# Optimization experiments

Measured on AMD Instinct MI355X. Metric: run time of the kernel, lower is better.

## Reference

```python
import jax, jax.numpy as jnp
import numpy as np

B, Q, K, D, H = 8, 1024, 1024, 1024, 16
HD = D // H
FFN = 4 * D


def layer_norm(x, w, b, eps=1e-5):
    mu = jnp.mean(x, axis=-1, keepdims=True)
    var = jnp.var(x, axis=-1, keepdims=True)
    return (x - mu) * jax.lax.rsqrt(var + eps) * w + b


def setup_inputs() -> dict:
    key = jax.random.key(0)
    ks = jax.random.split(key, 10)
    query = jax.random.normal(ks[0], (B, Q, D), dtype=jnp.float32)
    key_value = jax.random.normal(ks[1], (B, K, D), dtype=jnp.float32)
    kpm = jax.random.randint(ks[2], (B, K), 0, 2).astype(bool)
    kpm = kpm.at[:, 0].set(True)  # guarantee >=1 valid key per row
    s = 0.02
    return {
        "query": query,
        "key_value": key_value,
        "key_padding_mask": kpm,
        "ln_q_w": jnp.ones((D,), jnp.float32), "ln_q_b": jnp.zeros((D,), jnp.float32),
        "ln_kv_w": jnp.ones((D,), jnp.float32), "ln_kv_b": jnp.zeros((D,), jnp.float32),
        "ln_f_w": jnp.ones((D,), jnp.float32), "ln_f_b": jnp.zeros((D,), jnp.float32),
        "in_proj_w": jax.random.normal(ks[3], (3 * D, D), jnp.float32) * s,
        "in_proj_b": jnp.zeros((3 * D,), jnp.float32),
        "out_proj_w": jax.random.normal(ks[4], (D, D), jnp.float32) * s,
        "out_proj_b": jnp.zeros((D,), jnp.float32),
        "ffn_w1": jax.random.normal(ks[5], (FFN, D), jnp.float32) * s,
        "ffn_b1": jnp.zeros((FFN,), jnp.float32),
        "ffn_w2": jax.random.normal(ks[6], (D, FFN), jnp.float32) * s,
        "ffn_b2": jnp.zeros((D,), jnp.float32),
    }


def reference(query, key_value, key_padding_mask,
              ln_q_w, ln_q_b, ln_kv_w, ln_kv_b, ln_f_w, ln_f_b,
              in_proj_w, in_proj_b, out_proj_w, out_proj_b,
              ffn_w1, ffn_b1, ffn_w2, ffn_b2):
    q_norm = layer_norm(query, ln_q_w, ln_q_b)
    kv_norm = layer_norm(key_value, ln_kv_w, ln_kv_b)

    Wq, Wk, Wv = jnp.split(in_proj_w, 3, axis=0)
    bq, bk, bv = jnp.split(in_proj_b, 3, axis=0)
    q = (q_norm @ Wq.T + bq).reshape(B, Q, H, HD).transpose(0, 2, 1, 3)  # (B,H,Q,hd)
    k = (kv_norm @ Wk.T + bk).reshape(B, K, H, HD).transpose(0, 2, 1, 3)
    v = (kv_norm @ Wv.T + bv).reshape(B, K, H, HD).transpose(0, 2, 1, 3)

    scale = 1.0 / jnp.sqrt(jnp.float32(HD))
    scores = jnp.einsum('bhqd,bhkd->bhqk', q * scale, k)  # (B,H,Q,K)
    scores = jnp.where(key_padding_mask[:, None, None, :], scores, -jnp.inf)
    attn = jax.nn.softmax(scores, axis=-1)

    attn_out = jnp.einsum('bhqk,bhkd->bhqd', attn, v)
    attn_out = attn_out.transpose(0, 2, 1, 3).reshape(B, Q, D)
    attn_out = attn_out @ out_proj_w.T + out_proj_b

    x = query + attn_out
    h = layer_norm(x, ln_f_w, ln_f_b)
    h = jax.nn.gelu(h @ ffn_w1.T + ffn_b1, approximate=False)
    x = x + (h @ ffn_w2.T + ffn_b2)

    attn_weights = jnp.mean(attn, axis=1)  # average over heads -> (B,Q,K)
    return x, attn_weights
```

## Files before the change

### kernel.cpp

```cpp
#include <hip/hip_runtime.h>
#include <math.h>

typedef short  s16x8 __attribute__((ext_vector_type(8)));
typedef short  s16x4 __attribute__((ext_vector_type(4)));
typedef float  f32x4 __attribute__((ext_vector_type(4)));

#define DEV static __device__ __forceinline__
#define M0SHIFT 3.0f

DEV float b2f(unsigned short h) {
    unsigned int u = ((unsigned int)h) << 16;
    float f; __builtin_memcpy(&f, &u, 4); return f;
}
DEV unsigned short f2b(float f) {
    unsigned int u; __builtin_memcpy(&u, &f, 4);
    unsigned int r = (u + 0x7fffu + ((u >> 16) & 1u)) >> 16;
    return (unsigned short)r;
}
DEV unsigned fb(float x) { unsigned u; __builtin_memcpy(&u, &x, 4); return u; }
DEV s16x4 pack4(float a0, float a1, float a2, float a3) {
    unsigned lo = __builtin_amdgcn_perm(fb(a1), fb(a0), 0x07060302u);
    unsigned hi = __builtin_amdgcn_perm(fb(a3), fb(a2), 0x07060302u);
    unsigned long long p = ((unsigned long long)hi << 32) | lo;
    s16x4 r; __builtin_memcpy(&r, &p, 8); return r;
}

#define GLD16(gp, lp) __builtin_amdgcn_global_load_lds( \
    (const __attribute__((address_space(1))) unsigned int*)(const void*)(gp), \
    (__attribute__((address_space(3))) unsigned int*)(void*)(lp), 16, 0, 0)

#if __has_builtin(__builtin_amdgcn_mfma_f32_16x16x16_bf16)
#define MFMA16(a, b, c) __builtin_amdgcn_mfma_f32_16x16x16_bf16(a, b, c, 0, 0, 0)
#else
#define MFMA16(a, b, c) __builtin_amdgcn_mfma_f32_16x16x16bf16_1k(a, b, c, 0, 0, 0)
#endif

DEV float ldsel(const void* p, size_t i, bool f32) {
    return f32 ? ((const float*)p)[i] : b2f(((const unsigned short*)p)[i]);
}
DEV s16x8 ld8sel(const void* p, size_t eidx, bool f32) {
    if (f32) {
        const float* f = (const float*)p + eidx;
        f32x4 a = *(const f32x4*)f;
        f32x4 b = *(const f32x4*)(f + 4);
        s16x8 o;
        o[0]=(short)f2b(a[0]); o[1]=(short)f2b(a[1]); o[2]=(short)f2b(a[2]); o[3]=(short)f2b(a[3]);
        o[4]=(short)f2b(b[0]); o[5]=(short)f2b(b[1]); o[6]=(short)f2b(b[2]); o[7]=(short)f2b(b[3]);
        return o;
    }
    return *(const s16x8*)((const unsigned short*)p + eidx);
}

__global__ __launch_bounds__(256) void dtype_probe(
    const unsigned int* __restrict__ q, int* __restrict__ flag)
{
    int t = threadIdx.x;
    int hits = 0;
    for (int i = t; i < 2048; i += 256) {
        unsigned e0 = (q[i] >> 7) & 0xFFu;
        hits += (e0 >= 0x70u && e0 <= 0x87u) ? 1 : 0;
    }
#pragma unroll
    for (int m = 32; m >= 1; m >>= 1) hits += __shfl_xor(hits, m);
    __shared__ int sh[4];
    if ((t & 63) == 0) sh[t >> 6] = hits;
    __syncthreads();
    if (t == 0) *flag = (sh[0] + sh[1] + sh[2] + sh[3] > 1024) ? 0 : 1;
}

__global__ __launch_bounds__(1024) void mask_prep(
    const unsigned int* __restrict__ w, const unsigned char* __restrict__ bytes,
    float* __restrict__ mf)
{
    __shared__ int flag;
    const int t = threadIdx.x;
    if (t == 0) flag = 0;
    __syncthreads();
    unsigned int a = w[t], b = w[t + 1024];
    if (a > 1u || b > 1u) flag = 1;
    __syncthreads();
    const int f = flag;
    const float NEGINF = -__builtin_inff();
#pragma unroll
    for (int i = 0; i < 8; i++) {
        int c = t * 8 + i;
        int v = f ? (int)(bytes[c] != 0) : (int)(w[c] != 0);
        mf[c] = v ? -M0SHIFT : NEGINF;
    }
}

struct CvtArgs { const void* s[8]; };
__global__ __launch_bounds__(256) void cvt_w(
    const int* __restrict__ flagp, CvtArgs a, unsigned short* __restrict__ dst)
{
    const int f = *flagp;
    size_t e = ((size_t)blockIdx.x * 256 + threadIdx.x) * 8;
    if (e >= 12592128u) return;
    const size_t off[9] = {0u, 3145728u, 4194304u, 8388608u, 12582912u,
                           12585984u, 12587008u, 12591104u, 12592128u};
    int s = 0;
    while (e >= off[s + 1]) s++;
    *(s16x8*)&dst[e] = ld8sel(a.s[s], e - off[s], f == 1);
}

__global__ __launch_bounds__(256) void ln_k(
    const int* __restrict__ flagp, int xmode, int wmode,
    const void* __restrict__ x1p, const void* __restrict__ w1p, const void* __restrict__ b1p,
    unsigned short* __restrict__ y1p,
    const void* __restrict__ x2p, const void* __restrict__ w2p, const void* __restrict__ b2p,
    unsigned short* __restrict__ y2p)
{
    const int f = *flagp;
    const bool xf = (xmode == 2) ? (f == 1) : (xmode == 1);
    const bool wf = (wmode == 2) ? (f == 1) : (wmode == 1);
    int row = blockIdx.x;
    const void* x = x1p; const void* wgt = w1p; const void* bias = b1p;
    unsigned short* y = y1p;
    if (x2p && row >= 8192) {
        row -= 8192; x = x2p; wgt = w2p; bias = b2p; y = y2p;
    }
    const int t = threadIdx.x;
    const int w = t >> 6, lane = t & 63;
    float f0, f1, f2, f3;
    if (xf) {
        f32x4 v = *(const f32x4*)((const float*)x + (size_t)row * 1024 + t * 4);
        f0 = v[0]; f1 = v[1]; f2 = v[2]; f3 = v[3];
    } else {
        s16x4 v = *(const s16x4*)((const unsigned short*)x + (size_t)row * 1024 + t * 4);
        f0 = b2f((unsigned short)v[0]); f1 = b2f((unsigned short)v[1]);
        f2 = b2f((unsigned short)v[2]); f3 = b2f((unsigned short)v[3]);
    }
    __shared__ float red[4];
    float s = f0 + f1 + f2 + f3;
#pragma unroll
    for (int m = 32; m >= 1; m >>= 1) s += __shfl_xor(s, m);
    if (lane == 0) red[w] = s;
    __syncthreads();
    float mu = (red[0] + red[1] + red[2] + red[3]) * (1.0f / 1024.0f);
    float d0 = f0 - mu, d1 = f1 - mu, d2 = f2 - mu, d3 = f3 - mu;
    float q = d0 * d0 + d1 * d1 + d2 * d2 + d3 * d3;
#pragma unroll
    for (int m = 32; m >= 1; m >>= 1) q += __shfl_xor(q, m);
    __syncthreads();
    if (lane == 0) red[w] = q;
    __syncthreads();
    float var = (red[0] + red[1] + red[2] + red[3]) * (1.0f / 1024.0f);
    float rs = rsqrtf(var + 1e-5f);
    s16x4 vo;
    vo[0] = (short)f2b(d0 * rs * ldsel(wgt, t*4+0, wf) + ldsel(bias, t*4+0, wf));
    vo[1] = (short)f2b(d1 * rs * ldsel(wgt, t*4+1, wf) + ldsel(bias, t*4+1, wf));
    vo[2] = (short)f2b(d2 * rs * ldsel(wgt, t*4+2, wf) + ldsel(bias, t*4+2, wf));
    vo[3] = (short)f2b(d3 * rs * ldsel(wgt, t*4+3, wf) + ldsel(bias, t*4+3, wf));
    *(s16x4*)&y[(size_t)row * 1024 + t * 4] = vo;
}

__global__ __launch_bounds__(256) void gemm_bt(
    const int* __restrict__ flagp,
    const unsigned short* __restrict__ A,
    const void* __restrict__ W, size_t woff, int wmode,
    const void* __restrict__ bias, size_t boff, int bmode,
    const void* __restrict__ res, int rmode,
    void* __restrict__ C, int omode,
    int M, int N, int Kd, int ldw, int ldc, int act)
{
    const int f = *flagp;
    const bool wf = (wmode == 2) && (f == 1);
    __shared__ alignas(16) unsigned short As[128 * 32];
    __shared__ alignas(16) unsigned short Bs[128 * 32];
    const int t = threadIdx.x;
    const int m0 = blockIdx.y * 128, n0 = blockIdx.x * 128;
    const int w = t >> 6, lane = t & 63, quad = lane >> 4, l16 = lane & 15;
    const int wm = (w >> 1) * 64, wn = (w & 1) * 64;
    const f32x4 zero = {0.f, 0.f, 0.f, 0.f};
    f32x4 acc[4][4];
#pragma unroll
    for (int i = 0; i < 4; i++)
#pragma unroll
        for (int j = 0; j < 4; j++) acc[i][j] = zero;
    const int r0 = t >> 2, c0 = (t & 3) * 8;
    unsigned short* AsW = As + (size_t)w * 512;
    unsigned short* BsW = Bs + (size_t)w * 512;
    const unsigned short* W16 = (const unsigned short*)W + woff;
    const float*          W32 = (const float*)W + woff;

    for (int kt = 0; kt < Kd; kt += 32) {
        GLD16(&A[(size_t)(m0 + r0) * Kd + kt + c0],      AsW);
        GLD16(&A[(size_t)(m0 + r0 + 64) * Kd + kt + c0], AsW + 2048);
        if (wf) {
            *(s16x8*)&Bs[r0 * 32 + c0]        = ld8sel(W32, (size_t)(n0 + r0) * ldw + kt + c0, true);
            *(s16x8*)&Bs[(r0 + 64) * 32 + c0] = ld8sel(W32, (size_t)(n0 + r0 + 64) * ldw + kt + c0, true);
        } else {
            GLD16(&W16[(size_t)(n0 + r0) * ldw + kt + c0],      BsW);
            GLD16(&W16[(size_t)(n0 + r0 + 64) * ldw + kt + c0], BsW + 2048);
        }
        __syncthreads();
        s16x8 af[4], bfr[4];
#pragma unroll
        for (int i = 0; i < 4; i++) {
            af[i]  = *(const s16x8*)&As[(wm + i * 16 + l16) * 32 + quad * 8];
            bfr[i] = *(const s16x8*)&Bs[(wn + i * 16 + l16) * 32 + quad * 8];
        }
#pragma unroll
        for (int mi = 0; mi < 4; mi++)
#pragma unroll
            for (int ni = 0; ni < 4; ni++)
                acc[mi][ni] = __builtin_amdgcn_mfma_f32_16x16x32_bf16(af[mi], bfr[ni], acc[mi][ni], 0, 0, 0);
        __syncthreads();
    }
    const bool bf = (bmode == 2) && (f == 1);
    const bool rf = (rmode == 2) || (rmode == 3 && f == 1);
    const bool of = (omode == 1) || (omode == 2 && f == 1);
#pragma unroll
    for (int mi = 0; mi < 4; mi++)
#pragma unroll
        for (int ni = 0; ni < 4; ni++)
#pragma unroll
            for (int r = 0; r < 4; r++) {
                int gr = m0 + wm + mi * 16 + quad * 4 + r;
                int gc = n0 + wn + ni * 16 + l16;
                float v = acc[mi][ni][r];
                if (bmode >= 0) v += ldsel(bias, boff + gc, bf);
                if (act) v = 0.5f * v * (1.f + erff(v * 0.70710678118f));
                if (rmode) v += ldsel(res, (size_t)gr * ldc + gc, rf);
                size_t ci = (size_t)gr * ldc + gc;
                if (of) ((float*)C)[ci] = v;
                else ((unsigned short*)C)[ci] = f2b(v);
            }
}

__global__ __launch_bounds__(512, 2) void gemm8(
    const unsigned short* __restrict__ A,
    const unsigned short* __restrict__ W, size_t woff,
    const unsigned short* __restrict__ bias, size_t boff,
    unsigned short* __restrict__ C,
    int Kd, int ldc, int act)
{
    __shared__ alignas(16) unsigned short lds[65536];
    const unsigned short* Wp = W + woff;
    const int t = threadIdx.x;
    const int w = t >> 6, lane = t & 63, quad = lane >> 4, l16 = lane & 15;
    const int wr = w >> 2, wcn = w & 3;

    const int gx = (int)gridDim.x;
    const int nwg = gx * (int)gridDim.y;
    const int lid = (int)blockIdx.y * gx + (int)blockIdx.x;
    const int swz = (lid & 7) * (nwg >> 3) + (lid >> 3);
    const int m0 = (swz / gx) * 256, n0 = (swz % gx) * 256;

    const int hrow = w * 16 + (lane >> 3);
    const int scol = ((lane & 7) ^ ((lane & 32) ? 2 : 0)) * 8;
    const int NT = Kd >> 6;

    const int swq = (l16 & 4) ? 16 : 0;
    const int ck0 = (quad * 8) ^ swq;
    const int ck1 = (32 + quad * 8) ^ swq;

    const f32x4 zero = {0.f, 0.f, 0.f, 0.f};
    f32x4 acc[8][4];
#pragma unroll
    for (int i = 0; i < 8; i++)
#pragma unroll
        for (int j = 0; j < 4; j++) acc[i][j] = zero;
    s16x8 aF[4][2], bLo[2][2], bHi[2][2];

#define SA8(bb,h,tt,g) GLD16(&A[(size_t)(m0 + (h)*128 + hrow + (g)*8) * Kd + (size_t)(tt)*64 + scol], \
                             &lds[(bb)*32768 + (h)*8192 + (w*16 + (g)*8)*64])
#define SB8(bb,h,tt,g) GLD16(&Wp[(size_t)(n0 + (h)*128 + hrow + (g)*8) * Kd + (size_t)(tt)*64 + scol], \
                             &lds[(bb)*32768 + 16384 + (h)*8192 + (w*16 + (g)*8)*64])
#define LDA8(bb,q) { _Pragma("unroll") for (int i_ = 0; i_ < 4; i_++) { \
        const int ar_ = (q)*128 + wr*64 + i_*16 + l16; \
        aF[i_][0] = *(const s16x8*)&lds[(bb)*32768 + ar_*64 + ck0]; \
        aF[i_][1] = *(const s16x8*)&lds[(bb)*32768 + ar_*64 + ck1]; } }
#define LDB8(bb,dst,q) { _Pragma("unroll") for (int j_ = 0; j_ < 2; j_++) { \
        const int br_ = (q)*128 + wcn*32 + j_*16 + l16; \
        dst[j_][0] = *(const s16x8*)&lds[(bb)*32768 + 16384 + br_*64 + ck0]; \
        dst[j_][1] = *(const s16x8*)&lds[(bb)*32768 + 16384 + br_*64 + ck1]; } }
#define MM8(mq,nq,bsrc) { __builtin_amdgcn_s_setprio(1); \
        _Pragma("unroll") for (int i_ = 0; i_ < 4; i_++) \
        _Pragma("unroll") for (int j_ = 0; j_ < 2; j_++) { \
            acc[(mq)*4+i_][(nq)*2+j_] = __builtin_amdgcn_mfma_f32_16x16x32_bf16(aF[i_][0], bsrc[j_][0], acc[(mq)*4+i_][(nq)*2+j_], 0, 0, 0); \
            acc[(mq)*4+i_][(nq)*2+j_] = __builtin_amdgcn_mfma_f32_16x16x32_bf16(aF[i_][1], bsrc[j_][1], acc[(mq)*4+i_][(nq)*2+j_], 0, 0, 0); } \
        __builtin_amdgcn_s_setprio(0); }
#define BAR8() __builtin_amdgcn_s_barrier()
#define VMW8(n) asm volatile("s_waitcnt vmcnt(" #n ")" ::: "memory")

    SA8(0, 0, 0, 0); SA8(0, 0, 0, 1);
    SB8(0, 0, 0, 0); SB8(0, 0, 0, 1);
    SB8(0, 1, 0, 0); SB8(0, 1, 0, 1);
    SA8(0, 1, 0, 0); SA8(0, 1, 0, 1);
    VMW8(4); BAR8();

    for (int tt = 0; tt < NT - 1; tt++) {
        const int bb = tt & 1, nb = bb ^ 1;
        SA8(nb, 0, tt + 1, 0); SA8(nb, 0, tt + 1, 1);
        LDA8(bb, 0); LDB8(bb, bLo, 0);
        MM8(0, 0, bLo);
        VMW8(4); BAR8();
        SB8(nb, 0, tt + 1, 0); SB8(nb, 0, tt + 1, 1);
        LDB8(bb, bHi, 1);
        MM8(0, 1, bHi);
        VMW8(4); BAR8();
        SB8(nb, 1, tt + 1, 0); SB8(nb, 1, tt + 1, 1);
        LDA8(bb, 1);
        MM8(1, 1, bHi);
        BAR8();
        SA8(nb, 1, tt + 1, 0); SA8(nb, 1, tt + 1, 1);
        MM8(1, 0, bLo);
        VMW8(4); BAR8();
    }
    {
        const int bb = (NT - 1) & 1;
        LDA8(bb, 0); LDB8(bb, bLo, 0); MM8(0, 0, bLo); VMW8(2); BAR8();
        LDB8(bb, bHi, 1);              MM8(0, 1, bHi); VMW8(0); BAR8();
        LDA8(bb, 1);                   MM8(1, 1, bHi);
        MM8(1, 0, bLo);
    }

#pragma unroll
    for (int nq = 0; nq < 2; nq++)
#pragma unroll
    for (int j = 0; j < 2; j++) {
        const int gc = n0 + nq * 128 + wcn * 32 + j * 16 + l16;
        const float bv = b2f(bias[boff + gc]);
#pragma unroll
        for (int mq = 0; mq < 2; mq++)
#pragma unroll
        for (int i = 0; i < 4; i++)
#pragma unroll
        for (int r = 0; r < 4; r++) {
            const int gr = m0 + mq * 128 + wr * 64 + i * 16 + quad * 4 + r;
            float v = acc[mq * 4 + i][nq * 2 + j][r] + bv;
            if (act) v = 0.5f * v * (1.f + erff(v * 0.70710678118f));
            C[(size_t)gr * ldc + gc] = f2b(v);
        }
    }
#undef SA8
#undef SB8
#undef LDA8
#undef LDB8
#undef MM8
#undef BAR8
#undef VMW8
}

__global__ __launch_bounds__(256) void repack_kv(
    const unsigned short* __restrict__ kvp,
    unsigned short* __restrict__ kf, unsigned short* __restrict__ vf)
{
    const bool isv = blockIdx.x >= 4096;
    int t = (blockIdx.x - (isv ? 4096 : 0)) * 256 + threadIdx.x;
    int lane = t & 63;
    int quad = lane >> 4, l16 = lane & 15;
    if (!isv) {
        int half = (t >> 6) & 1, tile = (t >> 7) & 63;
        int h = (t >> 13) & 15, b = t >> 17;
        s16x8 v = *(const s16x8*)&kvp[(size_t)(b * 1024 + tile * 16 + l16) * 2048
                                      + h * 64 + half * 32 + quad * 8];
        *(s16x8*)&kf[(size_t)t * 8] = v;
    } else {
        int dt = (t >> 6) & 3, kt5 = (t >> 8) & 31;
        int h = (t >> 13) & 15, b = t >> 17;
        int d = dt * 16 + l16;
        s16x8 o;
#pragma unroll
        for (int j = 0; j < 8; j++) {
            int k = kt5 * 32 + ((j < 4) ? (quad * 4 + j) : (16 + quad * 4 + j - 4));
            o[j] = (short)kvp[(size_t)(b * 1024 + k) * 2048 + 1024 + h * 64 + d];
        }
        *(s16x8*)&vf[(size_t)t * 8] = o;
    }
}

__global__ __launch_bounds__(256) void flash_attn(
    const unsigned short* __restrict__ qp, const unsigned short* __restrict__ kf,
    const unsigned short* __restrict__ vf, const float* __restrict__ maskf,
    unsigned short* __restrict__ ao, float* __restrict__ ml)
{
    const int bh = blockIdx.x;
    const int b = bh >> 4, h = bh & 15;
    const int t = threadIdx.x, w = t >> 6, lane = t & 63, quad = lane >> 4, l16 = lane & 15;
    const int q0 = (blockIdx.y * 4 + w) * 16;
    const f32x4 zero = {0.f, 0.f, 0.f, 0.f};

    const unsigned short* kfb = kf + (size_t)bh * 65536;
    const unsigned short* vfb = vf + (size_t)bh * 65536;

    const size_t qbase = (size_t)(b * 1024 + q0 + l16) * 1024 + h * 64 + quad * 8;
    s16x8 qf0 = *(const s16x8*)&qp[qbase];
    s16x8 qf1 = *(const s16x8*)&qp[qbase + 32];

    f32x4 O[4];
#pragma unroll
    for (int dt = 0; dt < 4; dt++) O[dt] = zero;
    float l_s = 0.f;

    for (int kt = 0; kt < 1024; kt += 32) {
        const int tile2 = (kt >> 4) * 2;
        s16x8 k00 = *(const s16x8*)&kfb[(size_t)(tile2 + 0) * 512 + lane * 8];
        s16x8 k01 = *(const s16x8*)&kfb[(size_t)(tile2 + 1) * 512 + lane * 8];
        s16x8 k10 = *(const s16x8*)&kfb[(size_t)(tile2 + 2) * 512 + lane * 8];
        s16x8 k11 = *(const s16x8*)&kfb[(size_t)(tile2 + 3) * 512 + lane * 8];
        f32x4 St0 = __builtin_amdgcn_mfma_f32_16x16x32_bf16(k00, qf0, zero, 0, 0, 0);
        St0 = __builtin_amdgcn_mfma_f32_16x16x32_bf16(k01, qf1, St0, 0, 0, 0);
        f32x4 St1 = __builtin_amdgcn_mfma_f32_16x16x32_bf16(k10, qf0, zero, 0, 0, 0);
        St1 = __builtin_amdgcn_mfma_f32_16x16x32_bf16(k11, qf1, St1, 0, 0, 0);

        f32x4 mk0 = *(const f32x4*)&maskf[b * 1024 + kt + quad * 4];
        f32x4 mk1 = *(const f32x4*)&maskf[b * 1024 + kt + 16 + quad * 4];
        float x0[4], x1[4];
#pragma unroll
        for (int r = 0; r < 4; r++) {
            x0[r] = __expf(St0[r] * 0.125f + mk0[r]);
            x1[r] = __expf(St1[r] * 0.125f + mk1[r]);
        }
        float rs = (x0[0] + x0[1]) + (x0[2] + x0[3])
                 + (x1[0] + x1[1]) + (x1[2] + x1[3]);
        rs += __shfl_xor(rs, 16);
        rs += __shfl_xor(rs, 32);
        l_s += rs;

        s16x4 p0 = pack4(x0[0], x0[1], x0[2], x0[3]);
        s16x4 p1 = pack4(x1[0], x1[1], x1[2], x1[3]);
        const size_t vrow = (size_t)(kt >> 5) * 4;
#pragma unroll
        for (int dt = 0; dt < 4; dt++) {
            s16x8 vv = *(const s16x8*)&vfb[(vrow + dt) * 512 + lane * 8];
            s16x4 v0 = {vv[0], vv[1], vv[2], vv[3]};
            s16x4 v1 = {vv[4], vv[5], vv[6], vv[7]};
            O[dt] = MFMA16(p0, v0, O[dt]);
            O[dt] = MFMA16(p1, v1, O[dt]);
        }
    }
    float li = (l_s > 0.f) ? 1.f / l_s : 0.f;
    float lib[4];
#pragma unroll
    for (int r = 0; r < 4; r++) lib[r] = __shfl(li, quad * 4 + r);
#pragma unroll
    for (int dt = 0; dt < 4; dt++)
#pragma unroll
        for (int r = 0; r < 4; r++) {
            int qrow = q0 + quad * 4 + r;
            ao[(size_t)(b * 1024 + qrow) * 1024 + h * 64 + dt * 16 + l16] = f2b(O[dt][r] * lib[r]);
        }
    if (lane < 16) {
        size_t ix = ((size_t)(b * 16 + h) * 1024 + q0 + l16) * 2;
        ml[ix] = M0SHIFT; ml[ix + 1] = l_s;
    }
}

__global__ __launch_bounds__(256) void attn_mean_k(
    const int* __restrict__ flagp,
    const unsigned short* __restrict__ qp, const unsigned short* __restrict__ kf,
    const float* __restrict__ maskf, const float* __restrict__ ml,
    void* __restrict__ dout)
{
    const bool of = (*flagp == 1);
    const size_t SHIFT = (size_t)8 * 1024 * 1024;
    const int b = blockIdx.x, q0 = blockIdx.y * 16;
    const int t = threadIdx.x, w = t >> 6, lane = t & 63, quad = lane >> 4, l16 = lane & 15;
    const int kbase = w * 256;
    const f32x4 zero = {0.f, 0.f, 0.f, 0.f};
    f32x4 acc[16];
#pragma unroll
    for (int i = 0; i < 16; i++) acc[i] = zero;
    float mka[16];
#pragma unroll
    for (int i = 0; i < 16; i++)
        mka[i] = maskf[b * 1024 + kbase + i * 16 + l16];
    for (int h = 0; h < 16; h++) {
        const size_t qb = (size_t)(b * 1024 + q0 + l16) * 1024 + h * 64 + quad * 8;
        s16x8 a0 = *(const s16x8*)&qp[qb];
        s16x8 a1 = *(const s16x8*)&qp[qb + 32];
        float cexp[4], lirow[4];
#pragma unroll
        for (int r = 0; r < 4; r++) {
            size_t ix = ((size_t)(b * 16 + h) * 1024 + q0 + quad * 4 + r) * 2;
            float lv = ml[ix + 1];
            cexp[r] = M0SHIFT - ml[ix];
            lirow[r] = (lv > 0.f) ? 1.f / lv : 0.f;
        }
        const unsigned short* kfb = kf + ((size_t)(b * 16 + h) * 128 + (kbase >> 4) * 2) * 512;
#pragma unroll
        for (int i = 0; i < 16; i++) {
            s16x8 b0 = *(const s16x8*)&kfb[(size_t)(i * 2 + 0) * 512 + lane * 8];
            s16x8 b1 = *(const s16x8*)&kfb[(size_t)(i * 2 + 1) * 512 + lane * 8];
            f32x4 S = __builtin_amdgcn_mfma_f32_16x16x32_bf16(a0, b0, zero, 0, 0, 0);
            S = __builtin_amdgcn_mfma_f32_16x16x32_bf16(a1, b1, S, 0, 0, 0);
#pragma unroll
            for (int r = 0; r < 4; r++)
                acc[i][r] += __expf(S[r] * 0.125f + mka[i] + cexp[r]) * lirow[r];
        }
    }
#pragma unroll
    for (int i = 0; i < 16; i++)
#pragma unroll
        for (int r = 0; r < 4; r++) {
            int qrow = q0 + quad * 4 + r;
            size_t oi = SHIFT + (size_t)(b * 1024 + qrow) * 1024 + kbase + i * 16 + l16;
            float v = acc[i][r] * 0.0625f;
            if (of) ((float*)dout)[oi] = v;
            else ((unsigned short*)dout)[oi] = f2b(v);
        }
}

extern "C" void kernel_launch(void* const* d_in, const int* in_sizes, int n_in,
                              void* d_out, int out_size, void* d_ws, size_t ws_size,
                              hipStream_t stream) {
    const void* query = d_in[0];
    const void* keyv  = d_in[1];
    const void* maskr = d_in[2];
    const void* lqw = d_in[3];  const void* lqb = d_in[4];
    const void* lkw = d_in[5];  const void* lkb = d_in[6];
    const void* lfw = d_in[7];  const void* lfb = d_in[8];
    const void* ipw = d_in[9];  const void* ipb = d_in[10];
    const void* opw = d_in[11]; const void* opb = d_in[12];
    const void* w1  = d_in[13]; const void* b1  = d_in[14];
    const void* w2  = d_in[15]; const void* b2  = d_in[16];

    char* ws = (char*)d_ws;
    const size_t MB = 1024 * 1024;
    unsigned short* qn  = (unsigned short*)(ws + 0 * MB);
    unsigned short* kvn = (unsigned short*)(ws + 16 * MB);
    unsigned short* qpj = (unsigned short*)(ws + 32 * MB);
    unsigned short* kvp = (unsigned short*)(ws + 48 * MB);
    unsigned short* kfr = (unsigned short*)(ws + 80 * MB);
    unsigned short* vfr = (unsigned short*)(ws + 16 * MB);
    float*          ml  = (float*)(ws + 96 * MB);
    int*            fl  = (int*)(ws + 97 * MB);
    float*          mf  = (float*)(ws + 97 * MB + 256 * 1024);
    unsigned short* aco = (unsigned short*)(ws + 0 * MB);
    float*          xbf = (float*)(ws + 16 * MB);
    unsigned short* hn  = (unsigned short*)(ws + 48 * MB);
    unsigned short* g   = (unsigned short*)(ws + 64 * MB);
    unsigned short* wc  = (unsigned short*)(ws + 98 * MB);

    const bool big = ws_size >= (size_t)125 * MB;
    const size_t cWq = 0, cWk = 1048576, cWo = 3145728;
    const size_t cW1 = 4194304, cW2 = 8388608;
    const size_t cBq = 12582912, cBo = 12585984, cB1 = 12587008, cB2 = 12591104;

    const void *Wq, *Wk, *Wo, *Wf1, *Wf2, *Bq, *Bo, *Bf1, *Bf2;
    size_t wq_o, wk_o, wo_o, w1_o, w2_o, bq_o, bk_o, bo_o, b1_o, b2_o;
    int wm, bm;
    if (big) {
        Wq = Wk = Wo = Wf1 = Wf2 = Bq = Bo = Bf1 = Bf2 = wc;
        wq_o = cWq; wk_o = cWk; wo_o = cWo; w1_o = cW1; w2_o = cW2;
        bq_o = cBq; bk_o = cBq + 1024; bo_o = cBo; b1_o = cB1; b2_o = cB2;
        wm = 0; bm = 0;
    } else {
        Wq = Wk = ipw; Wo = opw; Wf1 = w1; Wf2 = w2;
        Bq = ipb; Bo = opb; Bf1 = b1; Bf2 = b2;
        wq_o = 0; wk_o = 1048576; wo_o = 0; w1_o = 0; w2_o = 0;
        bq_o = 0; bk_o = 1024; bo_o = 0; b1_o = 0; b2_o = 0;
        wm = 2; bm = 2;
    }

    dtype_probe<<<1, 256, 0, stream>>>((const unsigned int*)query, fl);
    mask_prep<<<1, 1024, 0, stream>>>((const unsigned int*)maskr, (const unsigned char*)maskr, mf);
    if (big) {
        CvtArgs ca; ca.s[0] = ipw; ca.s[1] = opw; ca.s[2] = w1; ca.s[3] = w2;
        ca.s[4] = ipb; ca.s[5] = opb; ca.s[6] = b1; ca.s[7] = b2;
        cvt_w<<<6149, 256, 0, stream>>>(fl, ca, wc);
    }

    ln_k<<<16384, 256, 0, stream>>>(fl, 2, 2, query, lqw, lqb, qn, keyv, lkw, lkb, kvn);

    gemm_bt<<<dim3(8, 64), 256, 0, stream>>>(fl, qn,  Wq, wq_o, wm, Bq, bq_o, bm,
                                             nullptr, 0, qpj, 0, 8192, 1024, 1024, 1024, 1024, 0);
    if (big) {
        gemm8<<<dim3(8, 32), 512, 0, stream>>>(kvn, wc, wk_o, wc, bk_o,
                                               kvp, 1024, 2048, 0);
    } else {
        gemm_bt<<<dim3(16, 64), 256, 0, stream>>>(fl, kvn, Wk, wk_o, wm, Bq, bk_o, bm,
                                                  nullptr, 0, kvp, 0, 8192, 2048, 1024, 1024, 2048, 0);
    }

    repack_kv<<<8192, 256, 0, stream>>>(kvp, kfr, vfr);
    flash_attn<<<dim3(128, 16), 256, 0, stream>>>(qpj, kfr, vfr, mf, aco, ml);
    attn_mean_k<<<dim3(8, 64), 256, 0, stream>>>(fl, qpj, kfr, mf, ml, d_out);

    gemm_bt<<<dim3(8, 64), 256, 0, stream>>>(fl, aco, Wo, wo_o, wm, Bo, bo_o, bm,
                                             query, 3, xbf, 1, 8192, 1024, 1024, 1024, 1024, 0);
    ln_k<<<8192, 256, 0, stream>>>(fl, 1, 2, xbf, lfw, lfb, hn,
                                   nullptr, nullptr, nullptr, nullptr);

    if (big) {
        gemm8<<<dim3(8, 32), 512, 0, stream>>>(hn, wc, w1_o, wc, b1_o,
                                               g, 1024, 2048, 1);
    } else {
        gemm_bt<<<dim3(16, 64), 256, 0, stream>>>(fl, hn, Wf1, w1_o, wm, Bf1, b1_o, bm,
                                                  nullptr, 0, g, 0, 8192, 2048, 1024, 1024, 2048, 1);
    }
    gemm_bt<<<dim3(8, 64), 256, 0, stream>>>(fl, g, Wf2, w2_o, wm, Bf2, b2_o, bm,
                                             xbf, 2, xbf, 1, 8192, 1024, 2048, 4096, 1024, 0);
    if (big) {
        gemm8<<<dim3(8, 32), 512, 0, stream>>>(hn, wc, w1_o + (size_t)2048 * 1024, wc, b1_o + 2048,
                                               g, 1024, 2048, 1);
    } else {
        gemm_bt<<<dim3(16, 64), 256, 0, stream>>>(fl, hn, Wf1, w1_o + (size_t)2048 * 1024, wm,
                                                  Bf1, b1_o + 2048, bm,
                                                  nullptr, 0, g, 0, 8192, 2048, 1024, 1024, 2048, 1);
    }
    gemm_bt<<<dim3(8, 64), 256, 0, stream>>>(fl, g, Wf2, w2_o + 2048, wm,
                                             nullptr, 0, -1,
                                             xbf, 2, d_out, 2, 8192, 1024, 2048, 4096, 1024, 0);
}
```

Before: 812.5 us.

## Process two query tiles per wave in flash attention and use exp2

```diff
diff --git a/kernel.cpp b/kernel.cpp
--- a/kernel.cpp
+++ b/kernel.cpp
@@ -7,6 +7,14 @@
 
 #define DEV static __device__ __forceinline__
 #define M0SHIFT 3.0f
+#define LOG2E   1.44269504088896f
+#define SCL2F   0.18033688011112f
+
+#if __has_builtin(__builtin_amdgcn_exp2f)
+#define EXP2F(x) __builtin_amdgcn_exp2f(x)
+#else
+#define EXP2F(x) exp2f(x)
+#endif
 
 DEV float b2f(unsigned short h) {
     unsigned int u = ((unsigned int)h) << 16;
@@ -85,7 +93,7 @@
     for (int i = 0; i < 8; i++) {
         int c = t * 8 + i;
         int v = f ? (int)(bytes[c] != 0) : (int)(w[c] != 0);
-        mf[c] = v ? -M0SHIFT : NEGINF;
+        mf[c] = v ? (-M0SHIFT * LOG2E) : NEGINF;
     }
 }
 
@@ -371,7 +379,7 @@
     }
 }
 
-__global__ __launch_bounds__(256) void flash_attn(
+__global__ __launch_bounds__(256, 4) void flash_attn(
     const unsigned short* __restrict__ qp, const unsigned short* __restrict__ kf,
     const unsigned short* __restrict__ vf, const float* __restrict__ maskf,
     unsigned short* __restrict__ ao, float* __restrict__ ml)
@@ -379,20 +387,21 @@
     const int bh = blockIdx.x;
     const int b = bh >> 4, h = bh & 15;
     const int t = threadIdx.x, w = t >> 6, lane = t & 63, quad = lane >> 4, l16 = lane & 15;
-    const int q0 = (blockIdx.y * 4 + w) * 16;
+    const int q0 = (blockIdx.y * 4 + w) * 32;
     const f32x4 zero = {0.f, 0.f, 0.f, 0.f};
 
     const unsigned short* kfb = kf + (size_t)bh * 65536;
     const unsigned short* vfb = vf + (size_t)bh * 65536;
 
-    const size_t qbase = (size_t)(b * 1024 + q0 + l16) * 1024 + h * 64 + quad * 8;
-    s16x8 qf0 = *(const s16x8*)&qp[qbase];
-    s16x8 qf1 = *(const s16x8*)&qp[qbase + 32];
-
-    f32x4 O[4];
-#pragma unroll
-    for (int dt = 0; dt < 4; dt++) O[dt] = zero;
-    float l_s = 0.f;
+    const size_t qbA = (size_t)(b * 1024 + q0 + l16) * 1024 + h * 64 + quad * 8;
+    const size_t qbB = qbA + (size_t)16 * 1024;
+    s16x8 qa0 = *(const s16x8*)&qp[qbA], qa1 = *(const s16x8*)&qp[qbA + 32];
+    s16x8 qb0 = *(const s16x8*)&qp[qbB], qb1 = *(const s16x8*)&qp[qbB + 32];
+
+    f32x4 OA[4], OB[4];
+#pragma unroll
+    for (int dt = 0; dt < 4; dt++) { OA[dt] = zero; OB[dt] = zero; }
+    float lsA = 0.f, lsB = 0.f;
 
     for (int kt = 0; kt < 1024; kt += 32) {
         const int tile2 = (kt >> 4) * 2;
@@ -400,51 +409,73 @@
         s16x8 k01 = *(const s16x8*)&kfb[(size_t)(tile2 + 1) * 512 + lane * 8];
         s16x8 k10 = *(const s16x8*)&kfb[(size_t)(tile2 + 2) * 512 + lane * 8];
         s16x8 k11 = *(const s16x8*)&kfb[(size_t)(tile2 + 3) * 512 + lane * 8];
-        f32x4 St0 = __builtin_amdgcn_mfma_f32_16x16x32_bf16(k00, qf0, zero, 0, 0, 0);
-        St0 = __builtin_amdgcn_mfma_f32_16x16x32_bf16(k01, qf1, St0, 0, 0, 0);
-        f32x4 St1 = __builtin_amdgcn_mfma_f32_16x16x32_bf16(k10, qf0, zero, 0, 0, 0);
-        St1 = __builtin_amdgcn_mfma_f32_16x16x32_bf16(k11, qf1, St1, 0, 0, 0);
+        const size_t vrow = (size_t)(kt >> 5) * 4;
+        s16x8 vv[4];
+#pragma unroll
+        for (int dt = 0; dt < 4; dt++)
+            vv[dt] = *(const s16x8*)&vfb[(vrow + dt) * 512 + lane * 8];
+
+        f32x4 SA0 = __builtin_amdgcn_mfma_f32_16x16x32_bf16(k00, qa0, zero, 0, 0, 0);
+        SA0 = __builtin_amdgcn_mfma_f32_16x16x32_bf16(k01, qa1, SA0, 0, 0, 0);
+        f32x4 SA1 = __builtin_amdgcn_mfma_f32_16x16x32_bf16(k10, qa0, zero, 0, 0, 0);
+        SA1 = __builtin_amdgcn_mfma_f32_16x16x32_bf16(k11, qa1, SA1, 0, 0, 0);
+        f32x4 SB0 = __builtin_amdgcn_mfma_f32_16x16x32_bf16(k00, qb0, zero, 0, 0, 0);
+        SB0 = __builtin_amdgcn_mfma_f32_16x16x32_bf16(k01, qb1, SB0, 0, 0, 0);
+        f32x4 SB1 = __builtin_amdgcn_mfma_f32_16x16x32_bf16(k10, qb0, zero, 0, 0, 0);
+        SB1 = __builtin_amdgcn_mfma_f32_16x16x32_bf16(k11, qb1, SB1, 0, 0, 0);
 
         f32x4 mk0 = *(const f32x4*)&maskf[b * 1024 + kt + quad * 4];
         f32x4 mk1 = *(const f32x4*)&maskf[b * 1024 + kt + 16 + quad * 4];
-        float x0[4], x1[4];
+        float xA0[4], xA1[4], xB0[4], xB1[4];
 #pragma unroll
         for (int r = 0; r < 4; r++) {
-            x0[r] = __expf(St0[r] * 0.125f + mk0[r]);
-            x1[r] = __expf(St1[r] * 0.125f + mk1[r]);
-        }
-        float rs = (x0[0] + x0[1]) + (x0[2] + x0[3])
-                 + (x1[0] + x1[1]) + (x1[2] + x1[3]);
-        rs += __shfl_xor(rs, 16);
-        rs += __shfl_xor(rs, 32);
-        l_s += rs;
-
-        s16x4 p0 = pack4(x0[0], x0[1], x0[2], x0[3]);
-        s16x4 p1 = pack4(x1[0], x1[1], x1[2], x1[3]);
-        const size_t vrow = (size_t)(kt >> 5) * 4;
+            xA0[r] = EXP2F(SA0[r] * SCL2F + mk0[r]);
+            xA1[r] = EXP2F(SA1[r] * SCL2F + mk1[r]);
+            xB0[r] = EXP2F(SB0[r] * SCL2F + mk0[r]);
+            xB1[r] = EXP2F(SB1[r] * SCL2F + mk1[r]);
+        }
+        float rsA = (xA0[0] + xA0[1]) + (xA0[2] + xA0[3])
+                  + (xA1[0] + xA1[1]) + (xA1[2] + xA1[3]);
+        float rsB = (xB0[0] + xB0[1]) + (xB0[2] + xB0[3])
+                  + (xB1[0] + xB1[1]) + (xB1[2] + xB1[3]);
+        rsA += __shfl_xor(rsA, 16);  rsA += __shfl_xor(rsA, 32);
+        rsB += __shfl_xor(rsB, 16);  rsB += __shfl_xor(rsB, 32);
+        lsA += rsA;  lsB += rsB;
+
+        s16x4 pA0 = pack4(xA0[0], xA0[1], xA0[2], xA0[3]);
+        s16x4 pA1 = pack4(xA1[0], xA1[1], xA1[2], xA1[3]);
+        s16x4 pB0 = pack4(xB0[0], xB0[1], xB0[2], xB0[3]);
+        s16x4 pB1 = pack4(xB1[0], xB1[1], xB1[2], xB1[3]);
 #pragma unroll
         for (int dt = 0; dt < 4; dt++) {
-            s16x8 vv = *(const s16x8*)&vfb[(vrow + dt) * 512 + lane * 8];
-            s16x4 v0 = {vv[0], vv[1], vv[2], vv[3]};
-            s16x4 v1 = {vv[4], vv[5], vv[6], vv[7]};
-            O[dt] = MFMA16(p0, v0, O[dt]);
-            O[dt] = MFMA16(p1, v1, O[dt]);
-        }
-    }
-    float li = (l_s > 0.f) ? 1.f / l_s : 0.f;
-    float lib[4];
-#pragma unroll
-    for (int r = 0; r < 4; r++) lib[r] = __shfl(li, quad * 4 + r);
+            s16x4 v0 = {vv[dt][0], vv[dt][1], vv[dt][2], vv[dt][3]};
+            s16x4 v1 = {vv[dt][4], vv[dt][5], vv[dt][6], vv[dt][7]};
+            OA[dt] = MFMA16(pA0, v0, OA[dt]);
+            OA[dt] = MFMA16(pA1, v1, OA[dt]);
+            OB[dt] = MFMA16(pB0, v0, OB[dt]);
+            OB[dt] = MFMA16(pB1, v1, OB[dt]);
+        }
+    }
+    float liA = (lsA > 0.f) ? 1.f / lsA : 0.f;
+    float liB = (lsB > 0.f) ? 1.f / lsB : 0.f;
+    float libA[4], libB[4];
+#pragma unroll
+    for (int r = 0; r < 4; r++) {
+        libA[r] = __shfl(liA, quad * 4 + r);
+        libB[r] = __shfl(liB, quad * 4 + r);
+    }
 #pragma unroll
     for (int dt = 0; dt < 4; dt++)
 #pragma unroll
         for (int r = 0; r < 4; r++) {
-            int qrow = q0 + quad * 4 + r;
-            ao[(size_t)(b * 1024 + qrow) * 1024 + h * 64 + dt * 16 + l16] = f2b(O[dt][r] * lib[r]);
+            int qrA = q0 + quad * 4 + r;
+            ao[(size_t)(b * 1024 + qrA) * 1024 + h * 64 + dt * 16 + l16] = f2b(OA[dt][r] * libA[r]);
+            ao[(size_t)(b * 1024 + qrA + 16) * 1024 + h * 64 + dt * 16 + l16] = f2b(OB[dt][r] * libB[r]);
         }
     if (lane < 16) {
         size_t ix = ((size_t)(b * 16 + h) * 1024 + q0 + l16) * 2;
-        ml[ix] = M0SHIFT; ml[ix + 1] = l_s;
+        ml[ix] = M0SHIFT;      ml[ix + 1] = lsA;
+        ml[ix + 32] = M0SHIFT; ml[ix + 33] = lsB;
     }
 }
 
@@ -476,7 +507,7 @@
         for (int r = 0; r < 4; r++) {
             size_t ix = ((size_t)(b * 16 + h) * 1024 + q0 + quad * 4 + r) * 2;
             float lv = ml[ix + 1];
-            cexp[r] = M0SHIFT - ml[ix];
+            cexp[r] = (M0SHIFT - ml[ix]) * LOG2E;
             lirow[r] = (lv > 0.f) ? 1.f / lv : 0.f;
         }
         const unsigned short* kfb = kf + ((size_t)(b * 16 + h) * 128 + (kbase >> 4) * 2) * 512;
@@ -488,7 +519,7 @@
             S = __builtin_amdgcn_mfma_f32_16x16x32_bf16(a1, b1, S, 0, 0, 0);
 #pragma unroll
             for (int r = 0; r < 4; r++)
-                acc[i][r] += __expf(S[r] * 0.125f + mka[i] + cexp[r]) * lirow[r];
+                acc[i][r] += EXP2F(S[r] * SCL2F + mka[i] + cexp[r]) * lirow[r];
         }
     }
 #pragma unroll
@@ -576,7 +607,7 @@
     }
 
     repack_kv<<<8192, 256, 0, stream>>>(kvp, kfr, vfr);
-    flash_attn<<<dim3(128, 16), 256, 0, stream>>>(qpj, kfr, vfr, mf, aco, ml);
+    flash_attn<<<dim3(128, 8), 256, 0, stream>>>(qpj, kfr, vfr, mf, aco, ml);
     attn_mean_k<<<dim3(8, 64), 256, 0, stream>>>(fl, qpj, kfr, mf, ml, d_out);
 
     gemm_bt<<<dim3(8, 64), 256, 0, stream>>>(fl, aco, Wo, wo_o, wm, Bo, bo_o, bm,
```

Measured after the change: 779.3 us. -4.1%, faster.
